# Optimization experiments

Measured on AMD Instinct MI355X. Metric: run time of the kernel, lower is better.

## Reference

```python
import jax, jax.numpy as jnp
import numpy as np

B, C, H, W = 8, 128, 256, 256
KERNELS = [1, 3, 5]


def _dwconv(x, w, k):
    # depthwise conv, groups == channels, padding k//2 (SAME for odd k)
    return jax.lax.conv_general_dilated(
        x, w, window_strides=(1, 1),
        padding=[(k // 2, k // 2), (k // 2, k // 2)],
        dimension_numbers=("NCHW", "OIHW", "NCHW"),
        feature_group_count=x.shape[1])


def setup_inputs() -> dict:
    key = jax.random.key(0)
    ks = jax.random.split(key, 5)
    x = jax.random.normal(ks[0], (B, C, H, W), jnp.float32)
    # depthwise weights: torch layout [out_ch, in_ch/groups, k, k] = [4C, 1, k, k]
    w1 = jax.random.normal(ks[1], (4 * C, 1, 1, 1), jnp.float32) * 0.2
    w3 = jax.random.normal(ks[2], (4 * C, 1, 3, 3), jnp.float32) * 0.1
    w5 = jax.random.normal(ks[3], (4 * C, 1, 5, 5), jnp.float32) * 0.05
    # proj 1x1 conv: [4C, 12C, 1, 1]
    w_proj = jax.random.normal(ks[4], (4 * C, 12 * C, 1, 1), jnp.float32) * 0.02
    return {"x": x, "w1": w1, "w3": w3, "w5": w5, "w_proj": w_proj}


def reference(x, w1, w3, w5, w_proj):
    # DWT: strided split -> channel concat  [B,C,H,W] -> [B,4C,H/2,W/2]
    xd = jnp.concatenate([
        x[:, :, 0::2, 0::2], x[:, :, 0::2, 1::2],
        x[:, :, 1::2, 0::2], x[:, :, 1::2, 1::2]], axis=1)
    # multi-kernel depthwise convs, concat -> [B,12C,H/2,W/2]
    feats = jnp.concatenate([
        _dwconv(xd, w1, 1), _dwconv(xd, w3, 3), _dwconv(xd, w5, 5)], axis=1)
    # 1x1 projection: [B,12C,h,w] -> [B,4C,h,w]
    y = jnp.einsum("bchw,oc->bohw", feats, w_proj[:, :, 0, 0])
    # IDWT: strided zero-scatter back to [B,C,H,W]
    c = y.shape[1] // 4
    ll, lh, hl, hh = jnp.split(y, 4, axis=1)
    out = jnp.zeros((y.shape[0], c, y.shape[2] * 2, y.shape[3] * 2), y.dtype)
    out = (out.at[:, :, 0::2, 0::2].set(ll)
              .at[:, :, 0::2, 1::2].set(lh)
              .at[:, :, 1::2, 0::2].set(hl)
              .at[:, :, 1::2, 1::2].set(hh))
    return out
```

## Files before the change

kernel.cpp:

```cpp
#include <hip/hip_runtime.h>
#include <hip/hip_bf16.h>
#include <stdint.h>

typedef __bf16 bf16_t;
typedef __bf16 bf16x8 __attribute__((ext_vector_type(8)));
typedef float f32x4 __attribute__((ext_vector_type(4)));

constexpr int CC = 128, HH = 256, WW = 256;
constexpr int C4 = 512, K12 = 1536;
constexpr int AWP_ELEMS = 786432;

__global__ __launch_bounds__(256)
void prep(const float* __restrict__ wp, const float* __restrict__ w1,
          const float* __restrict__ w3, const float* __restrict__ w5,
          bf16_t* __restrict__ awp, float* __restrict__ lwall)
{
    int t = blockIdx.x * 256 + threadIdx.x;
    if (t < AWP_ELEMS) {
        int kk = t & 31, o = (t >> 5) & 511, t2 = t >> 14;
        int g = t2 >> 4, cb = t2 & 15;
        awp[t] = (bf16_t)wp[o * K12 + g * C4 + cb * 32 + kk];
    }
    int u = t - AWP_ELEMS;
    if (u >= 0 && u < 512 * 36) {
        int c4 = u / 36, j = u - c4 * 36;
        float v = 0.f;
        if (j < 25)      v = w5[c4 * 25 + j];
        else if (j < 34) v = w3[c4 * 9 + (j - 25)];
        else if (j == 34) v = w1[c4];
        lwall[u] = v;
    }
}

__device__ __forceinline__ void gload4(const float* g, float* l) {
    __builtin_amdgcn_global_load_lds(
        (const __attribute__((address_space(1))) uint32_t*)g,
        (__attribute__((address_space(3))) uint32_t*)l, 4, 0, 0);
}

__device__ __forceinline__ uint32_t pk_bf16(float a, float b) {
    bf16_t x = (bf16_t)a, y = (bf16_t)b;
    return (uint32_t)__builtin_bit_cast(unsigned short, x)
         | ((uint32_t)__builtin_bit_cast(unsigned short, y) << 16);
}

__device__ __forceinline__ int bt_off(int row, int colbyte) {
    int f = ((row >> 1) ^ (row >> 2)) & 7;
    return row * 256 + (colbyte ^ (f << 4));
}

__global__ __launch_bounds__(512, 2)
void wtconv_mfma(const float* __restrict__ x,
                 const bf16_t* __restrict__ awp,
                 const float* __restrict__ lwall,
                 float* __restrict__ out)
{
    __shared__ __align__(16) float  lx[32][5][136];
    __shared__ __align__(16) char   BtB[128 * 256];
    __shared__ __align__(16) float  lw[2][32][36];

    const int tid = threadIdx.x;
    const int nb = blockIdx.x;
    const int m = (nb & 7) * 128 + (nb >> 3);
    const int b = m >> 7, i = m & 127;
    const int wave = tid >> 6, lane = tid & 63;
    const int wm = wave & 3, wn = wave >> 2;
    const int lrow = lane & 15, lkh = lane >> 4;
    const float* xb = x + (size_t)b * CC * HH * WW;

    for (int e = tid; e < 32 * 5 * 136 / 4; e += 512)
        ((f32x4*)lx)[e] = (f32x4){0.f, 0.f, 0.f, 0.f};
    __syncthreads();

    f32x4 acc[8][4];
#pragma unroll
    for (int a = 0; a < 8; ++a)
#pragma unroll
        for (int c = 0; c < 4; ++c) acc[a][c] = (f32x4){0.f, 0.f, 0.f, 0.f};

    auto issue_lx = [&](int cb) {
        const int q4 = cb >> 2;
        const int qy = q4 >> 1, qx = q4 & 1;
        const int bcb = (cb & 3) * 32;
#pragma unroll 1
        for (int t = 0; t < 40; ++t) {
            int q = wave * 40 + t;
            int chan = (q * 6554) >> 16;
            int rem = q - chan * 10;
            int r = rem >> 1, h = rem & 1;
            int ri = i + r - 2;
            if ((unsigned)ri < 128u) {
                const float* src = xb + (size_t)(bcb + chan) * (HH * WW)
                                 + (2 * ri + qy) * WW + 2 * (h * 64 + lane) + qx;
                gload4(src, &lx[chan][r][2 + h * 64]);
            }
        }
    };
    auto issue_lw = [&](int cb, int buf) {
        const float* src = lwall + cb * (32 * 36);
        float* dst = &lw[buf][0][0];
#pragma unroll 1
        for (int t = wave; t < 18; t += 8)
            gload4(src + t * 64 + lane, dst + t * 64);
    };

    issue_lw(0, 0);
    issue_lx(0);

    const int pxq = tid & 31, e = tid >> 5;
    const int px0 = pxq * 4;

#pragma unroll 1
    for (int cb = 0; cb < 16; ++cb) {
        __syncthreads();

        const int buf = cb & 1;
        float fw5[2][4], fw3[2][4], fw1[2][4];
#pragma unroll
        for (int cc = 0; cc < 2; ++cc) {
            const int chan = 2 * e + cc;
            f32x4 wv[9];
#pragma unroll
            for (int t = 0; t < 9; ++t)
                wv[t] = *(const f32x4*)&lw[buf][chan][t * 4];
#define WT(idx) (wv[(idx) >> 2][(idx) & 3])
            float f5[4] = {0.f, 0.f, 0.f, 0.f}, f3[4] = {0.f, 0.f, 0.f, 0.f}, f1[4];
#pragma unroll
            for (int r = 0; r < 5; ++r) {
                f32x4 a = *(const f32x4*)&lx[chan][r][px0];
                f32x4 bv = *(const f32x4*)&lx[chan][r][px0 + 4];
                float col[8] = {a[0], a[1], a[2], a[3], bv[0], bv[1], bv[2], bv[3]};
#pragma unroll
                for (int d = 0; d < 4; ++d)
#pragma unroll
                    for (int v = 0; v < 5; ++v)
                        f5[d] += WT(r * 5 + v) * col[d + v];
                if (r >= 1 && r <= 3) {
#pragma unroll
                    for (int d = 0; d < 4; ++d)
#pragma unroll
                        for (int v = 0; v < 3; ++v)
                            f3[d] += WT(25 + (r - 1) * 3 + v) * col[d + 1 + v];
                }
                if (r == 2) {
#pragma unroll
                    for (int d = 0; d < 4; ++d)
                        f1[d] = WT(34) * col[d + 2];
                }
            }
#undef WT
#pragma unroll
            for (int d = 0; d < 4; ++d) {
                fw5[cc][d] = f5[d]; fw3[cc][d] = f3[d]; fw1[cc][d] = f1[d];
            }
        }
#pragma unroll
        for (int d = 0; d < 4; ++d) {
            const int row = px0 + d;
            const int cbyte = e * 4;
            *(uint32_t*)&BtB[bt_off(row, cbyte)]        = pk_bf16(fw1[0][d], fw1[1][d]);
            *(uint32_t*)&BtB[bt_off(row, 64 + cbyte)]   = pk_bf16(fw3[0][d], fw3[1][d]);
            *(uint32_t*)&BtB[bt_off(row, 128 + cbyte)]  = pk_bf16(fw5[0][d], fw5[1][d]);
        }
        __syncthreads();

        if (cb < 15) { issue_lw(cb + 1, (cb + 1) & 1); issue_lx(cb + 1); }

#pragma unroll 1
        for (int g = 0; g < 3; ++g) {
            bf16x8 bfrag[4];
#pragma unroll
            for (int nf = 0; nf < 4; ++nf) {
                const int row = wn * 64 + nf * 16 + lrow;
                bfrag[nf] = *(const bf16x8*)&BtB[bt_off(row, g * 64 + lkh * 16)];
            }
            const bf16_t* abase = awp + (size_t)(g * 16 + cb) * (512 * 32);
#pragma unroll
            for (int mf = 0; mf < 8; ++mf) {
                const int o = wm * 128 + mf * 16 + lrow;
                bf16x8 af = *(const bf16x8*)(abase + o * 32 + lkh * 8);
#pragma unroll
                for (int nf = 0; nf < 4; ++nf)
                    acc[mf][nf] = __builtin_amdgcn_mfma_f32_16x16x32_bf16(
                        af, bfrag[nf], acc[mf][nf], 0, 0, 0);
            }
        }
    }

    const int oy = 2 * i + (wm >> 1);
    const int ox = wm & 1;
#pragma unroll
    for (int mf = 0; mf < 8; ++mf)
#pragma unroll
        for (int nf = 0; nf < 4; ++nf)
#pragma unroll
            for (int r = 0; r < 4; ++r) {
                int o  = wm * 128 + mf * 16 + lkh * 4 + r;
                int px = wn * 64 + nf * 16 + lrow;
                int bco = o & 127;
                out[((size_t)(b * CC + bco) * HH + oy) * WW + 2 * px + ox]
                    = acc[mf][nf][r];
            }
}

extern "C" void kernel_launch(void* const* d_in, const int* in_sizes, int n_in,
                              void* d_out, int out_size, void* d_ws, size_t ws_size,
                              hipStream_t stream) {
    const float* x  = (const float*)d_in[0];
    const float* w1 = (const float*)d_in[1];
    const float* w3 = (const float*)d_in[2];
    const float* w5 = (const float*)d_in[3];
    const float* wp = (const float*)d_in[4];
    float* out = (float*)d_out;
    bf16_t* awp  = (bf16_t*)d_ws;
    float* lwall = (float*)((char*)d_ws + (size_t)AWP_ELEMS * 2);

    int prep_total = AWP_ELEMS + 512 * 36;
    hipLaunchKernelGGL(prep, dim3((prep_total + 255) / 256), dim3(256), 0, stream,
                       wp, w1, w3, w5, awp, lwall);
    hipLaunchKernelGGL(wtconv_mfma, dim3(1024), dim3(512), 0, stream,
                       x, awp, lwall, out);
}
```

Before: 635.2 us.

## Double block to 1024 threads, one channel per thread, halve per-wave MFMA tile

Doubles the workgroup from 512 to 1024 threads (16 waves), so each wave owns half as many output rows in the GEMM (4x4 MFMA tiles instead of 8x4) and each thread computes depthwise convs for one channel instead of two. Depthwise weights are re-laid out as 5 rows of 8 so they load as aligned vec4 pairs, and the x tile loads are restructured to fixed per-wave channels with unrolled loops. The aim is more waves to hide latency and fewer accumulator registers per wave. The trade-off is that each A-fragment load from global now feeds fewer MFMAs, BtB stores become 16-bit writes, and a larger block may limit residency given the LDS footprint.

```diff
diff --git a/kernel.cpp b/kernel.cpp
--- a/kernel.cpp
+++ b/kernel.cpp
@@ -9,26 +9,29 @@
 constexpr int CC = 128, HH = 256, WW = 256;
 constexpr int C4 = 512, K12 = 1536;
 constexpr int AWP_ELEMS = 786432;
+constexpr int LW2_ELEMS = 512 * 40;
 
 __global__ __launch_bounds__(256)
 void prep(const float* __restrict__ wp, const float* __restrict__ w1,
           const float* __restrict__ w3, const float* __restrict__ w5,
-          bf16_t* __restrict__ awp, float* __restrict__ lwall)
+          bf16_t* __restrict__ awp, float* __restrict__ lw2g)
 {
     int t = blockIdx.x * 256 + threadIdx.x;
     if (t < AWP_ELEMS) {
         int kk = t & 31, o = (t >> 5) & 511, t2 = t >> 14;
         int g = t2 >> 4, cb = t2 & 15;
         awp[t] = (bf16_t)wp[o * K12 + g * C4 + cb * 32 + kk];
+        return;
     }
     int u = t - AWP_ELEMS;
-    if (u >= 0 && u < 512 * 36) {
-        int c4 = u / 36, j = u - c4 * 36;
-        float v = 0.f;
-        if (j < 25)      v = w5[c4 * 25 + j];
-        else if (j < 34) v = w3[c4 * 9 + (j - 25)];
-        else if (j == 34) v = w1[c4];
-        lwall[u] = v;
+    if (u < LW2_ELEMS) {
+        int c4 = u / 40, j = u - c4 * 40;
+        int r = j >> 3, v = j & 7;
+        float val = 0.f;
+        if (v < 5)                 val = w5[c4 * 25 + r * 5 + v];
+        else if (r >= 1 && r <= 3) val = w3[c4 * 9 + (r - 1) * 3 + (v - 5)];
+        else if (r == 0 && v == 5) val = w1[c4];
+        lw2g[u] = val;
     }
 }
 
@@ -38,43 +41,42 @@
         (__attribute__((address_space(3))) uint32_t*)l, 4, 0, 0);
 }
 
-__device__ __forceinline__ uint32_t pk_bf16(float a, float b) {
-    bf16_t x = (bf16_t)a, y = (bf16_t)b;
-    return (uint32_t)__builtin_bit_cast(unsigned short, x)
-         | ((uint32_t)__builtin_bit_cast(unsigned short, y) << 16);
-}
-
 __device__ __forceinline__ int bt_off(int row, int colbyte) {
     int f = ((row >> 1) ^ (row >> 2)) & 7;
     return row * 256 + (colbyte ^ (f << 4));
 }
 
-__global__ __launch_bounds__(512, 2)
+__device__ __forceinline__ uint16_t b16bits(float v) {
+    return __builtin_bit_cast(uint16_t, (bf16_t)v);
+}
+
+__global__ __launch_bounds__(1024, 4)
 void wtconv_mfma(const float* __restrict__ x,
                  const bf16_t* __restrict__ awp,
-                 const float* __restrict__ lwall,
+                 const float* __restrict__ lw2g,
                  float* __restrict__ out)
 {
-    __shared__ __align__(16) float  lx[32][5][136];
-    __shared__ __align__(16) char   BtB[128 * 256];
-    __shared__ __align__(16) float  lw[2][32][36];
+    __shared__ __align__(16) float lx[32][5][136];
+    __shared__ __align__(16) char  BtB[128 * 256];
+    __shared__ __align__(16) float lw2s[2][1280];
 
     const int tid = threadIdx.x;
+    const int lane = tid & 63;
+    const int wid = __builtin_amdgcn_readfirstlane(tid >> 6);
     const int nb = blockIdx.x;
     const int m = (nb & 7) * 128 + (nb >> 3);
     const int b = m >> 7, i = m & 127;
-    const int wave = tid >> 6, lane = tid & 63;
-    const int wm = wave & 3, wn = wave >> 2;
+    const int wm = wid & 7, wn = wid >> 3;
     const int lrow = lane & 15, lkh = lane >> 4;
     const float* xb = x + (size_t)b * CC * HH * WW;
 
-    for (int e = tid; e < 32 * 5 * 136 / 4; e += 512)
+    for (int e = tid; e < 32 * 5 * 136 / 4; e += 1024)
         ((f32x4*)lx)[e] = (f32x4){0.f, 0.f, 0.f, 0.f};
     __syncthreads();
 
-    f32x4 acc[8][4];
-#pragma unroll
-    for (int a = 0; a < 8; ++a)
+    f32x4 acc[4][4];
+#pragma unroll
+    for (int a = 0; a < 4; ++a)
 #pragma unroll
         for (int c = 0; c < 4; ++c) acc[a][c] = (f32x4){0.f, 0.f, 0.f, 0.f};
 
@@ -82,32 +84,36 @@
         const int q4 = cb >> 2;
         const int qy = q4 >> 1, qx = q4 & 1;
         const int bcb = (cb & 3) * 32;
-#pragma unroll 1
-        for (int t = 0; t < 40; ++t) {
-            int q = wave * 40 + t;
-            int chan = (q * 6554) >> 16;
-            int rem = q - chan * 10;
-            int r = rem >> 1, h = rem & 1;
-            int ri = i + r - 2;
-            if ((unsigned)ri < 128u) {
-                const float* src = xb + (size_t)(bcb + chan) * (HH * WW)
-                                 + (2 * ri + qy) * WW + 2 * (h * 64 + lane) + qx;
-                gload4(src, &lx[chan][r][2 + h * 64]);
+#pragma unroll
+        for (int cl = 0; cl < 2; ++cl) {
+            const int chan = wid * 2 + cl;
+#pragma unroll
+            for (int r = 0; r < 5; ++r) {
+                const int ri = i + r - 2;
+                if ((unsigned)ri < 128u) {
+#pragma unroll
+                    for (int h = 0; h < 2; ++h) {
+                        const float* s = xb + (((size_t)(bcb + chan)) << 16)
+                                       + (2 * ri + qy) * WW + qx + h * 128;
+                        gload4(s + 2 * lane, &lx[chan][r][2 + h * 64]);
+                    }
+                }
             }
         }
     };
     auto issue_lw = [&](int cb, int buf) {
-        const float* src = lwall + cb * (32 * 36);
-        float* dst = &lw[buf][0][0];
+        const float* src = lw2g + cb * 1280;
+        float* dst = lw2s[buf];
 #pragma unroll 1
-        for (int t = wave; t < 18; t += 8)
+        for (int t = wid; t < 20; t += 16)
             gload4(src + t * 64 + lane, dst + t * 64);
     };
 
     issue_lw(0, 0);
     issue_lx(0);
 
-    const int pxq = tid & 31, e = tid >> 5;
+    const int pxq = tid & 31;
+    const int chan = (tid >> 5) & 31;
     const int px0 = pxq * 4;
 
 #pragma unroll 1
@@ -115,52 +121,38 @@
         __syncthreads();
 
         const int buf = cb & 1;
-        float fw5[2][4], fw3[2][4], fw1[2][4];
-#pragma unroll
-        for (int cc = 0; cc < 2; ++cc) {
-            const int chan = 2 * e + cc;
-            f32x4 wv[9];
-#pragma unroll
-            for (int t = 0; t < 9; ++t)
-                wv[t] = *(const f32x4*)&lw[buf][chan][t * 4];
-#define WT(idx) (wv[(idx) >> 2][(idx) & 3])
-            float f5[4] = {0.f, 0.f, 0.f, 0.f}, f3[4] = {0.f, 0.f, 0.f, 0.f}, f1[4];
-#pragma unroll
-            for (int r = 0; r < 5; ++r) {
-                f32x4 a = *(const f32x4*)&lx[chan][r][px0];
-                f32x4 bv = *(const f32x4*)&lx[chan][r][px0 + 4];
-                float col[8] = {a[0], a[1], a[2], a[3], bv[0], bv[1], bv[2], bv[3]};
+        const float* wrow = &lw2s[buf][chan * 40];
+        float f5[4] = {0.f,0.f,0.f,0.f}, f3[4] = {0.f,0.f,0.f,0.f}, f1[4];
+        float w1v = 0.f;
+#pragma unroll
+        for (int r = 0; r < 5; ++r) {
+            f32x4 wA = *(const f32x4*)(wrow + r * 8);
+            f32x4 wB = *(const f32x4*)(wrow + r * 8 + 4);
+            f32x4 a  = *(const f32x4*)&lx[chan][r][px0];
+            f32x4 bv = *(const f32x4*)&lx[chan][r][px0 + 4];
+            float col[8] = {a[0],a[1],a[2],a[3],bv[0],bv[1],bv[2],bv[3]};
+            if (r == 0) w1v = wB[1];
+#pragma unroll
+            for (int d = 0; d < 4; ++d)
+                f5[d] += wA[0]*col[d] + wA[1]*col[d+1] + wA[2]*col[d+2]
+                       + wA[3]*col[d+3] + wB[0]*col[d+4];
+            if (r >= 1 && r <= 3) {
 #pragma unroll
                 for (int d = 0; d < 4; ++d)
-#pragma unroll
-                    for (int v = 0; v < 5; ++v)
-                        f5[d] += WT(r * 5 + v) * col[d + v];
-                if (r >= 1 && r <= 3) {
-#pragma unroll
-                    for (int d = 0; d < 4; ++d)
-#pragma unroll
-                        for (int v = 0; v < 3; ++v)
-                            f3[d] += WT(25 + (r - 1) * 3 + v) * col[d + 1 + v];
-                }
-                if (r == 2) {
-#pragma unroll
-                    for (int d = 0; d < 4; ++d)
-                        f1[d] = WT(34) * col[d + 2];
-                }
-            }
-#undef WT
-#pragma unroll
-            for (int d = 0; d < 4; ++d) {
-                fw5[cc][d] = f5[d]; fw3[cc][d] = f3[d]; fw1[cc][d] = f1[d];
+                    f3[d] += wB[1]*col[d+1] + wB[2]*col[d+2] + wB[3]*col[d+3];
+            }
+            if (r == 2) {
+#pragma unroll
+                for (int d = 0; d < 4; ++d) f1[d] = w1v * col[d + 2];
             }
         }
 #pragma unroll
         for (int d = 0; d < 4; ++d) {
             const int row = px0 + d;
-            const int cbyte = e * 4;
-            *(uint32_t*)&BtB[bt_off(row, cbyte)]        = pk_bf16(fw1[0][d], fw1[1][d]);
-            *(uint32_t*)&BtB[bt_off(row, 64 + cbyte)]   = pk_bf16(fw3[0][d], fw3[1][d]);
-            *(uint32_t*)&BtB[bt_off(row, 128 + cbyte)]  = pk_bf16(fw5[0][d], fw5[1][d]);
+            const int cby = chan * 2;
+            *(uint16_t*)&BtB[bt_off(row, cby)]       = b16bits(f1[d]);
+            *(uint16_t*)&BtB[bt_off(row, 64 + cby)]  = b16bits(f3[d]);
+            *(uint16_t*)&BtB[bt_off(row, 128 + cby)] = b16bits(f5[d]);
         }
         __syncthreads();
 
@@ -176,8 +168,8 @@
             }
             const bf16_t* abase = awp + (size_t)(g * 16 + cb) * (512 * 32);
 #pragma unroll
-            for (int mf = 0; mf < 8; ++mf) {
-                const int o = wm * 128 + mf * 16 + lrow;
+            for (int mf = 0; mf < 4; ++mf) {
+                const int o = wm * 64 + mf * 16 + lrow;
                 bf16x8 af = *(const bf16x8*)(abase + o * 32 + lkh * 8);
 #pragma unroll
                 for (int nf = 0; nf < 4; ++nf)
@@ -187,17 +179,16 @@
         }
     }
 
-    const int oy = 2 * i + (wm >> 1);
-    const int ox = wm & 1;
-#pragma unroll
-    for (int mf = 0; mf < 8; ++mf)
+    const int oy = 2 * i + (wm >> 2);
+    const int ox = (wm >> 1) & 1;
+#pragma unroll
+    for (int mf = 0; mf < 4; ++mf)
 #pragma unroll
         for (int nf = 0; nf < 4; ++nf)
 #pragma unroll
             for (int r = 0; r < 4; ++r) {
-                int o  = wm * 128 + mf * 16 + lkh * 4 + r;
-                int px = wn * 64 + nf * 16 + lrow;
-                int bco = o & 127;
+                const int bco = (wm & 1) * 64 + mf * 16 + lkh * 4 + r;
+                const int px  = wn * 64 + nf * 16 + lrow;
                 out[((size_t)(b * CC + bco) * HH + oy) * WW + 2 * px + ox]
                     = acc[mf][nf][r];
             }
@@ -212,12 +203,12 @@
     const float* w5 = (const float*)d_in[3];
     const float* wp = (const float*)d_in[4];
     float* out = (float*)d_out;
-    bf16_t* awp  = (bf16_t*)d_ws;
-    float* lwall = (float*)((char*)d_ws + (size_t)AWP_ELEMS * 2);
-
-    int prep_total = AWP_ELEMS + 512 * 36;
+    bf16_t* awp = (bf16_t*)d_ws;
+    float* lw2g = (float*)((char*)d_ws + (size_t)AWP_ELEMS * 2);
+
+    int prep_total = AWP_ELEMS + LW2_ELEMS;
     hipLaunchKernelGGL(prep, dim3((prep_total + 255) / 256), dim3(256), 0, stream,
-                       wp, w1, w3, w5, awp, lwall);
-    hipLaunchKernelGGL(wtconv_mfma, dim3(1024), dim3(512), 0, stream,
-                       x, awp, lwall, out);
-}
+                       wp, w1, w3, w5, awp, lw2g);
+    hipLaunchKernelGGL(wtconv_mfma, dim3(1024), dim3(1024), 0, stream,
+                       x, awp, lw2g, out);
+}
```

Result: faster. 536.8 us (-15.5%).
